# Optimization experiments

Measured on AMD Instinct MI355X. Metric: run time of the kernel, lower is better.

The kernel has to match this reference:

```python
import jax, jax.numpy as jnp
import numpy as np

N_EMBD = 1024
N_HEAD = 16
B, T = 8, 1024
EPS = 1e-5


def setup_inputs() -> dict:
    key = jax.random.key(0)
    ks = jax.random.split(key, 12)
    C = N_EMBD
    s_in = 1.0 / np.sqrt(C)
    s_ff = 1.0 / np.sqrt(4 * C)
    inp = {
        "x": jax.random.normal(ks[0], (B, T, C), dtype=jnp.float32),
        "mask": jnp.tril(jnp.ones((T, T), dtype=jnp.int32))[None, None, :, :],
        "ln1_w": jnp.ones((C,), jnp.float32),
        "ln1_b": jnp.zeros((C,), jnp.float32),
        "ln2_w": jnp.ones((C,), jnp.float32),
        "ln2_b": jnp.zeros((C,), jnp.float32),
        "wq": jax.random.normal(ks[1], (C, C), jnp.float32) * s_in,
        "bq": jnp.zeros((C,), jnp.float32),
        "wk": jax.random.normal(ks[2], (C, C), jnp.float32) * s_in,
        "bk": jnp.zeros((C,), jnp.float32),
        "wv": jax.random.normal(ks[3], (C, C), jnp.float32) * s_in,
        "bv": jnp.zeros((C,), jnp.float32),
        "wo": jax.random.normal(ks[4], (C, C), jnp.float32) * s_in,
        "bo": jnp.zeros((C,), jnp.float32),
        "w1": jax.random.normal(ks[5], (C, 4 * C), jnp.float32) * s_in,
        "b1": jnp.zeros((4 * C,), jnp.float32),
        "w2": jax.random.normal(ks[6], (4 * C, C), jnp.float32) * s_ff,
        "b2": jnp.zeros((C,), jnp.float32),
    }
    return inp


def _layer_norm(x, w, b):
    mu = jnp.mean(x, axis=-1, keepdims=True)
    var = jnp.mean(jnp.square(x - mu), axis=-1, keepdims=True)
    return (x - mu) * jax.lax.rsqrt(var + EPS) * w + b


def reference(x, mask, ln1_w, ln1_b, ln2_w, ln2_b,
              wq, bq, wk, bk, wv, bv, wo, bo, w1, b1, w2, b2):
    Bx, Tx, C = x.shape
    H = N_HEAD
    d = C // H
    h = _layer_norm(x, ln1_w, ln1_b)
    q = (h @ wq + bq).reshape(Bx, Tx, H, d)
    k = (h @ wk + bk).reshape(Bx, Tx, H, d)
    v = (h @ wv + bv).reshape(Bx, Tx, H, d)
    # [B,H,Tq,Tk] scores, scaled by sqrt(head_dim)
    scores = jnp.einsum('bqhd,bkhd->bhqk', q, k) / jnp.sqrt(jnp.float32(d))
    scores = jnp.where(mask == 0, -jnp.inf, scores)
    attn = jax.nn.softmax(scores, axis=-1)
    ctx = jnp.einsum('bhqk,bkhd->bqhd', attn, v).reshape(Bx, Tx, C)
    x = x + (ctx @ wo + bo)
    h2 = _layer_norm(x, ln2_w, ln2_b)
    ff = jax.nn.gelu(h2 @ w1 + b1, approximate=False) @ w2 + b2
    return x + ff
```

## Files before the change

kernel.cpp:

```cpp
#include <hip/hip_runtime.h>
#include <hip/hip_bf16.h>
#include <math.h>


#define DEVI __device__ __forceinline__

typedef __attribute__((ext_vector_type(4))) float floatx4;
typedef __attribute__((ext_vector_type(8))) short shortx8;

DEVI ushort f2b(float f) {
    __hip_bfloat16 h = __float2bfloat16(f);
    return __builtin_bit_cast(ushort, h);
}

DEVI void gl_lds16(const ushort* g, ushort* l) {
    __builtin_amdgcn_global_load_lds(
        (const __attribute__((address_space(1))) void*)g,
        (__attribute__((address_space(3))) void*)l, 16, 0, 0);
}

DEVI float gelu_f(float v) {
    const float u0 = 0.7978845608f * v * (1.0f + 0.044715f * v * v);
    const float u  = fminf(fmaxf(u0, -15.0f), 15.0f);
    const float e  = exp2f(u * 2.885390082f);
    const float th = 1.0f - 2.0f / (e + 1.0f);
    return 0.5f * v * (1.0f + th);
}

__global__ void transp4_kernel(const float* __restrict__ s0, const float* __restrict__ s1,
                               const float* __restrict__ s2, const float* __restrict__ s3,
                               ushort* __restrict__ d0, ushort* __restrict__ d1,
                               ushort* __restrict__ d2, ushort* __restrict__ d3) {
    const int z = blockIdx.z;
    const float* src = (z == 0) ? s0 : (z == 1) ? s1 : (z == 2) ? s2 : s3;
    ushort*      dst = (z == 0) ? d0 : (z == 1) ? d1 : (z == 2) ? d2 : d3;
    __shared__ float tile[32][33];
    const int c0 = blockIdx.x * 32, r0 = blockIdx.y * 32;
    const int tx = threadIdx.x, ty = threadIdx.y;
#pragma unroll
    for (int i = 0; i < 32; i += 8)
        tile[ty + i][tx] = src[(size_t)(r0 + ty + i) * 1024 + c0 + tx];
    __syncthreads();
#pragma unroll
    for (int i = 0; i < 32; i += 8)
        dst[(size_t)(c0 + ty + i) * 1024 + r0 + tx] = f2b(tile[tx][ty + i]);
}

__global__ void transp_kernel(const float* __restrict__ src,
                              ushort* __restrict__ dst, int R, int C) {
    __shared__ float tile[32][33];
    const int c0 = blockIdx.x * 32, r0 = blockIdx.y * 32;
    const int tx = threadIdx.x, ty = threadIdx.y;
#pragma unroll
    for (int i = 0; i < 32; i += 8)
        tile[ty + i][tx] = src[(size_t)(r0 + ty + i) * C + c0 + tx];
    __syncthreads();
#pragma unroll
    for (int i = 0; i < 32; i += 8)
        dst[(size_t)(c0 + ty + i) * R + r0 + tx] = f2b(tile[tx][ty + i]);
}

__global__ __launch_bounds__(256)
void ln_kernel(const float* __restrict__ x, const float* __restrict__ w,
               const float* __restrict__ b, ushort* __restrict__ out) {
    __shared__ float red[8];
    const int m = blockIdx.x;
    const int tid = threadIdx.x;
    const float4 xv = *(const float4*)&x[(size_t)m * 1024 + tid * 4];
    float s  = xv.x + xv.y + xv.z + xv.w;
    float s2 = xv.x * xv.x + xv.y * xv.y + xv.z * xv.z + xv.w * xv.w;
#pragma unroll
    for (int o = 32; o >= 1; o >>= 1) {
        s  += __shfl_xor(s, o, 64);
        s2 += __shfl_xor(s2, o, 64);
    }
    const int wv_ = tid >> 6;
    if ((tid & 63) == 0) { red[wv_] = s; red[4 + wv_] = s2; }
    __syncthreads();
    s  = red[0] + red[1] + red[2] + red[3];
    s2 = red[4] + red[5] + red[6] + red[7];
    const float mu   = s * (1.0f / 1024.0f);
    const float var  = s2 * (1.0f / 1024.0f) - mu * mu;
    const float rstd = rsqrtf(var + 1e-5f);
    const float4 wv = *(const float4*)&w[tid * 4];
    const float4 bv = *(const float4*)&b[tid * 4];
    ushort o4[4];
    o4[0] = f2b((xv.x - mu) * rstd * wv.x + bv.x);
    o4[1] = f2b((xv.y - mu) * rstd * wv.y + bv.y);
    o4[2] = f2b((xv.z - mu) * rstd * wv.z + bv.z);
    o4[3] = f2b((xv.w - mu) * rstd * wv.w + bv.w);
    *(uint2*)&out[(size_t)m * 1024 + tid * 4] = *(uint2*)o4;
}

template <int MODE>
__global__ __launch_bounds__(512, 4)
void gemmW(const ushort* __restrict__ A, const ushort* __restrict__ Bt,
           const float* __restrict__ biasQ, const float* __restrict__ biasK,
           const float* __restrict__ biasV,
           void* __restrict__ out, void* __restrict__ out2, void* __restrict__ out3,
           int N, int K) {
    __shared__ __align__(128) ushort lds[24576];

    const int tid  = threadIdx.x;
    const int lane = tid & 63;
    const int w    = tid >> 6;
    const int wr   = w >> 1;
    const int wc   = w & 1;

    int bx = blockIdx.x, by = blockIdx.y;
    {
        const int nwg = gridDim.x * gridDim.y;
        if ((nwg & 7) == 0) {
            const int flat = by * gridDim.x + bx;
            const int cpx  = nwg >> 3;
            const int wg   = (flat & 7) * cpx + (flat >> 3);
            bx = wg % gridDim.x;
            by = wg / gridDim.x;
        }
    }
    const int m0 = by * 256;
    const int n0 = bx * 128;

    floatx4 acc[4][4] = {};

    const int lr3 = lane >> 3;
    const int sc  = (lane & 7) ^ lr3;
    const ushort* pA = A  + (size_t)(m0 + w * 32 + lr3) * K + sc * 8;
    const ushort* pB = Bt + (size_t)(n0 + w * 16 + lr3) * K + sc * 8;
    ushort* sAd = lds + w * 2048;
    ushort* sBd = lds + 16384 + w * 1024;
    const size_t k8 = (size_t)8 * K, k16 = (size_t)16 * K, k24 = (size_t)24 * K;

    const int c0f  = (lane >> 4) ^ (lane & 7);
    const int aIdx = (wr * 64 + (lane & 15)) * 64 + c0f * 8;
    const int bIdx = (wc * 64 + (lane & 15)) * 64 + c0f * 8;
    const ushort* ar0 = lds + aIdx;
    const ushort* ar1 = lds + (aIdx ^ 32);
    const ushort* br0 = lds + 16384 + bIdx;
    const ushort* br1 = lds + 16384 + (bIdx ^ 32);

    for (int k0 = 0; k0 < K; k0 += 64) {
        __syncthreads();
        gl_lds16(pA + k0,       sAd);
        gl_lds16(pA + k8  + k0, sAd + 512);
        gl_lds16(pA + k16 + k0, sAd + 1024);
        gl_lds16(pA + k24 + k0, sAd + 1536);
        gl_lds16(pB + k0,       sBd);
        gl_lds16(pB + k8  + k0, sBd + 512);
        asm volatile("s_waitcnt vmcnt(0)" ::: "memory");
        __syncthreads();

        shortx8 af[4][2], bf[4][2];
#pragma unroll
        for (int mi = 0; mi < 4; ++mi) {
            af[mi][0] = *(const shortx8*)&ar0[mi * 1024];
            af[mi][1] = *(const shortx8*)&ar1[mi * 1024];
        }
#pragma unroll
        for (int ni = 0; ni < 4; ++ni) {
            bf[ni][0] = *(const shortx8*)&br0[ni * 1024];
            bf[ni][1] = *(const shortx8*)&br1[ni * 1024];
        }
#pragma unroll
        for (int mi = 0; mi < 4; ++mi)
#pragma unroll
            for (int ni = 0; ni < 4; ++ni) {
                acc[mi][ni] = __builtin_amdgcn_mfma_f32_16x16x32_bf16(
                    af[mi][0], bf[ni][0], acc[mi][ni], 0, 0, 0);
                acc[mi][ni] = __builtin_amdgcn_mfma_f32_16x16x32_bf16(
                    af[mi][1], bf[ni][1], acc[mi][ni], 0, 0, 0);
            }
    }
    __syncthreads();

    const int colL  = wc * 64 + (lane & 15);
    const int rbase = (wr & 1) * 64 + ((lane >> 4) << 2);
    const int mqme  = wr >> 1;

    if constexpr (MODE == 3) {
        float bvals[4];
#pragma unroll
        for (int ni = 0; ni < 4; ++ni) bvals[ni] = biasQ[n0 + colL + ni * 16];
        ushort* T = lds;
        ushort* o = (ushort*)out;
#pragma unroll
        for (int mq = 0; mq < 2; ++mq) {
            if (mqme == mq) {
#pragma unroll
                for (int mi = 0; mi < 4; ++mi)
#pragma unroll
                for (int ni = 0; ni < 4; ++ni) {
                    const int t0 = rbase + mi * 16;
#pragma unroll
                    for (int r = 0; r < 4; ++r)
                        T[(t0 + r) * 136 + colL + ni * 16] =
                            f2b(gelu_f(acc[mi][ni][r] + bvals[ni]));
                }
            }
            __syncthreads();
#pragma unroll
            for (int it = 0; it < 4; ++it) {
                const int idx = it * 512 + tid;
                const int row = idx >> 4, ch = idx & 15;
                const uint4 vv = *(const uint4*)&T[row * 136 + ch * 8];
                *(uint4*)&o[(size_t)(m0 + mq * 128 + row) * N + n0 + ch * 8] = vv;
            }
            __syncthreads();
        }
    }

    if constexpr (MODE == 1) {
        const int mat   = n0 >> 10;
        const int bb    = m0 >> 10;
        const int tbase = m0 & 1023;
        if (mat < 2) {
            const float* bp = (mat == 0) ? biasQ : biasK;
            ushort* dst = (mat == 0) ? (ushort*)out : (ushort*)out2;
            const int cb = n0 & 1023;
            float bvals[4];
#pragma unroll
            for (int ni = 0; ni < 4; ++ni) bvals[ni] = bp[cb + colL + ni * 16];
            ushort* T = lds;
#pragma unroll
            for (int mq = 0; mq < 2; ++mq) {
                if (mqme == mq) {
#pragma unroll
                    for (int mi = 0; mi < 4; ++mi)
#pragma unroll
                    for (int ni = 0; ni < 4; ++ni) {
                        const int t0 = rbase + mi * 16;
#pragma unroll
                        for (int r = 0; r < 4; ++r)
                            T[(t0 + r) * 136 + colL + ni * 16] =
                                f2b(acc[mi][ni][r] + bvals[ni]);
                    }
                }
                __syncthreads();
#pragma unroll
                for (int it = 0; it < 4; ++it) {
                    const int idx = it * 512 + tid;
                    const int row = idx >> 4, ch = idx & 15;
                    const uint4 vv = *(const uint4*)&T[row * 136 + ch * 8];
                    *(uint4*)&dst[(size_t)(m0 + mq * 128 + row) * 1024 + cb + ch * 8] = vv;
                }
                __syncthreads();
            }
        } else {
            const int vb = n0 - 2048;
            ushort* T = lds;
            ushort* Vt = (ushort*)out3;
            float bvals[4];
#pragma unroll
            for (int ni = 0; ni < 4; ++ni) bvals[ni] = biasV[vb + colL + ni * 16];
#pragma unroll
            for (int mq = 0; mq < 2; ++mq) {
                if (mqme == mq) {
#pragma unroll
                    for (int ni = 0; ni < 4; ++ni)
#pragma unroll
                    for (int mi = 0; mi < 4; ++mi) {
                        const int t0 = rbase + mi * 16;
#pragma unroll
                        for (int r = 0; r < 4; ++r)
                            T[(colL + ni * 16) * 136 + t0 + r] =
                                f2b(acc[mi][ni][r] + bvals[ni]);
                    }
                }
                __syncthreads();
#pragma unroll
                for (int it = 0; it < 4; ++it) {
                    const int idx = it * 512 + tid;
                    const int dim = idx >> 4, ch = idx & 15;
                    const uint4 vv = *(const uint4*)&T[dim * 136 + ch * 8];
                    const int d  = vb + dim;
                    const int hh = d >> 6, dl = d & 63;
                    *(uint4*)&Vt[((size_t)(bb * 16 + hh) * 64 + dl) * 1024
                                 + tbase + mq * 128 + ch * 8] = vv;
                }
                __syncthreads();
            }
        }
    }
}

__global__ __launch_bounds__(256, 4)
void gemm97r(const ushort* __restrict__ A, const ushort* __restrict__ Bt,
             const float* __restrict__ bias, float* __restrict__ out,
             const float* __restrict__ resid, int N, int K) {
    __shared__ __align__(128) ushort lds[18432];

    const int tid  = threadIdx.x;
    const int lane = tid & 63;
    const int w    = tid >> 6;
    const int wr   = w >> 1;
    const int wc   = w & 1;

    int bx = blockIdx.x, by = blockIdx.y;
    {
        const int nwg = gridDim.x * gridDim.y;
        if ((nwg & 7) == 0) {
            const int flat = by * gridDim.x + bx;
            const int cpx  = nwg >> 3;
            const int wg   = (flat & 7) * cpx + (flat >> 3);
            bx = wg % gridDim.x;
            by = wg / gridDim.x;
        }
    }
    const int m0 = by * 128;
    const int n0 = bx * 128;

    floatx4 acc[4][4] = {};

    const int lr3 = lane >> 3;
    const int sc  = (lane & 7) ^ lr3;
    const ushort* pA = A  + (size_t)(m0 + w * 32 + lr3) * K + sc * 8;
    const ushort* pB = Bt + (size_t)(n0 + w * 32 + lr3) * K + sc * 8;
    ushort* sAd = lds + w * 2048;
    ushort* sBd = lds + 8192 + w * 2048;
    const size_t k8 = (size_t)8 * K, k16 = (size_t)16 * K, k24 = (size_t)24 * K;

    const int c0f = (lane >> 4) ^ (lane & 7);
    const int aIdx = (wr * 64 + (lane & 15)) * 64 + c0f * 8;
    const int bIdx = (wc * 64 + (lane & 15)) * 64 + c0f * 8;
    const ushort* ar0 = lds + aIdx;
    const ushort* ar1 = lds + (aIdx ^ 32);
    const ushort* br0 = lds + 8192 + bIdx;
    const ushort* br1 = lds + 8192 + (bIdx ^ 32);

    for (int k0 = 0; k0 < K; k0 += 64) {
        __syncthreads();
        gl_lds16(pA + k0,       sAd);
        gl_lds16(pA + k8  + k0, sAd + 512);
        gl_lds16(pA + k16 + k0, sAd + 1024);
        gl_lds16(pA + k24 + k0, sAd + 1536);
        gl_lds16(pB + k0,       sBd);
        gl_lds16(pB + k8  + k0, sBd + 512);
        gl_lds16(pB + k16 + k0, sBd + 1024);
        gl_lds16(pB + k24 + k0, sBd + 1536);
        asm volatile("s_waitcnt vmcnt(0)" ::: "memory");
        __syncthreads();

        shortx8 af[4][2], bf[4][2];
#pragma unroll
        for (int mi = 0; mi < 4; ++mi) {
            af[mi][0] = *(const shortx8*)&ar0[mi * 1024];
            af[mi][1] = *(const shortx8*)&ar1[mi * 1024];
        }
#pragma unroll
        for (int ni = 0; ni < 4; ++ni) {
            bf[ni][0] = *(const shortx8*)&br0[ni * 1024];
            bf[ni][1] = *(const shortx8*)&br1[ni * 1024];
        }
#pragma unroll
        for (int mi = 0; mi < 4; ++mi)
#pragma unroll
            for (int ni = 0; ni < 4; ++ni) {
                acc[mi][ni] = __builtin_amdgcn_mfma_f32_16x16x32_bf16(
                    af[mi][0], bf[ni][0], acc[mi][ni], 0, 0, 0);
                acc[mi][ni] = __builtin_amdgcn_mfma_f32_16x16x32_bf16(
                    af[mi][1], bf[ni][1], acc[mi][ni], 0, 0, 0);
            }
    }
    __syncthreads();

    const int colL  = wc * 64 + (lane & 15);
    const int rbase = wr * 64 + ((lane >> 4) << 2);
    float bvals[4];
#pragma unroll
    for (int ni = 0; ni < 4; ++ni) bvals[ni] = bias[n0 + colL + ni * 16];
    float* T = (float*)lds;
    float* o = (float*)out;
#pragma unroll
    for (int half = 0; half < 2; ++half) {
        if (wr == half) {
#pragma unroll
            for (int mi = 0; mi < 4; ++mi)
#pragma unroll
            for (int ni = 0; ni < 4; ++ni) {
                const int t0 = mi * 16 + ((lane >> 4) << 2);
#pragma unroll
                for (int r = 0; r < 4; ++r)
                    T[(t0 + r) * 132 + colL + ni * 16] =
                        acc[mi][ni][r] + bvals[ni];
            }
        }
        __syncthreads();
#pragma unroll
        for (int it = 0; it < 8; ++it) {
            const int idx = it * 256 + tid;
            const int row = idx >> 5, ch = idx & 31;
            float4 tv = *(const float4*)&T[row * 132 + ch * 4];
            const size_t go = (size_t)(m0 + half * 64 + row) * N + n0 + ch * 4;
            const float4 rv = *(const float4*)&resid[go];
            tv.x += rv.x; tv.y += rv.y; tv.z += rv.z; tv.w += rv.w;
            *(float4*)&o[go] = tv;
        }
        __syncthreads();
    }
}

__global__ __launch_bounds__(256)
void attn_kernel(const ushort* __restrict__ Q, const ushort* __restrict__ Kk,
                 const ushort* __restrict__ Vt, ushort* __restrict__ ctx) {
    __shared__ ushort sK[64 * 64];
    __shared__ ushort sV[64 * 64];
    __shared__ ushort sP[4][16 * 72];

    const int tid  = threadIdx.x;
    const int lane = tid & 63;
    const int wave = tid >> 6;
    const int quad = lane >> 4;
    const int l15  = lane & 15;

    const int qb = 15 - (blockIdx.x >> 7);
    const int bh = blockIdx.x & 127;
    const size_t vbase = (size_t)bh << 16;
    const int bb = bh >> 4, h = bh & 15;

    const int lrow = lane >> 3;
    const int scb  = (lane & 7) ^ lrow;
    const ushort* Kg = Kk + ((size_t)bb * 1024 + wave * 8 + lrow) * 1024 + h * 64 + scb * 8;
    const ushort* Vg = Vt + vbase + (size_t)(wave * 8 + lrow) * 1024 + scb * 8;

    const int qrow = bb * 1024 + qb * 64 + wave * 16 + l15;
    const shortx8 qf0 = *(const shortx8*)&Q[(size_t)qrow * 1024 + h * 64 + quad * 8];
    const shortx8 qf1 = *(const shortx8*)&Q[(size_t)qrow * 1024 + h * 64 + 32 + quad * 8];

    const float SC = 0.125f * 1.44269504f;

    float mstate[4], lstate[4];
    floatx4 oacc[4] = {};
#pragma unroll
    for (int r = 0; r < 4; ++r) { mstate[r] = -__builtin_inff(); lstate[r] = 0.0f; }

    for (int kt = 0; kt <= qb; ++kt) {
        __syncthreads();
#pragma unroll
        for (int p = 0; p < 2; ++p) {
            gl_lds16(Kg + (size_t)kt * 65536 + (size_t)p * 32768,
                     sK + (p * 32 + wave * 8) * 64);
            gl_lds16(Vg + (size_t)kt * 64 + (size_t)p * 32 * 1024,
                     sV + (p * 32 + wave * 8) * 64);
        }
        __syncthreads();

        floatx4 s[4];
#pragma unroll
        for (int nt = 0; nt < 4; ++nt) {
            const int r = nt * 16 + l15;
            const int c0 = quad ^ (r & 7);
            const int c1 = (4 + quad) ^ (r & 7);
            const shortx8 kf0 = *(const shortx8*)&sK[r * 64 + c0 * 8];
            const shortx8 kf1 = *(const shortx8*)&sK[r * 64 + c1 * 8];
            floatx4 z = {};
            z = __builtin_amdgcn_mfma_f32_16x16x32_bf16(qf0, kf0, z, 0, 0, 0);
            z = __builtin_amdgcn_mfma_f32_16x16x32_bf16(qf1, kf1, z, 0, 0, 0);
            s[nt] = z;
        }
#pragma unroll
        for (int nt = 0; nt < 4; ++nt)
#pragma unroll
            for (int r = 0; r < 4; ++r) {
                float sv = s[nt][r] * SC;
                if (kt == qb) {
                    const int col = nt * 16 + l15;
                    const int row = wave * 16 + quad * 4 + r;
                    if (col > row) sv = -__builtin_inff();
                }
                s[nt][r] = sv;
            }
        float mnew[4], alpha[4];
#pragma unroll
        for (int r = 0; r < 4; ++r) {
            float mt = fmaxf(fmaxf(s[0][r], s[1][r]), fmaxf(s[2][r], s[3][r]));
#pragma unroll
            for (int o = 8; o >= 1; o >>= 1) mt = fmaxf(mt, __shfl_xor(mt, o, 64));
            mnew[r]  = fmaxf(mstate[r], mt);
            alpha[r] = exp2f(mstate[r] - mnew[r]);
            mstate[r] = mnew[r];
        }
#pragma unroll
        for (int r = 0; r < 4; ++r) {
            float rs = 0.0f;
#pragma unroll
            for (int nt = 0; nt < 4; ++nt) {
                const float p = exp2f(s[nt][r] - mnew[r]);
                s[nt][r] = p;
                rs += p;
            }
#pragma unroll
            for (int o = 8; o >= 1; o >>= 1) rs += __shfl_xor(rs, o, 64);
            lstate[r] = alpha[r] * lstate[r] + rs;
#pragma unroll
            for (int dt = 0; dt < 4; ++dt) oacc[dt][r] *= alpha[r];
        }
#pragma unroll
        for (int nt = 0; nt < 4; ++nt)
#pragma unroll
            for (int r = 0; r < 4; ++r)
                sP[wave][(quad * 4 + r) * 72 + nt * 16 + l15] = f2b(s[nt][r]);
        __asm__ volatile("s_waitcnt lgkmcnt(0)" ::: "memory");
        const shortx8 pf0 = *(const shortx8*)&sP[wave][l15 * 72 + quad * 8];
        const shortx8 pf1 = *(const shortx8*)&sP[wave][l15 * 72 + 32 + quad * 8];
#pragma unroll
        for (int dt = 0; dt < 4; ++dt) {
            const int r = dt * 16 + l15;
            const int c0 = quad ^ (r & 7);
            const int c1 = (4 + quad) ^ (r & 7);
            const shortx8 v0 = *(const shortx8*)&sV[r * 64 + c0 * 8];
            const shortx8 v1 = *(const shortx8*)&sV[r * 64 + c1 * 8];
            oacc[dt] = __builtin_amdgcn_mfma_f32_16x16x32_bf16(pf0, v0, oacc[dt], 0, 0, 0);
            oacc[dt] = __builtin_amdgcn_mfma_f32_16x16x32_bf16(pf1, v1, oacc[dt], 0, 0, 0);
        }
    }
#pragma unroll
    for (int dt = 0; dt < 4; ++dt)
#pragma unroll
        for (int r = 0; r < 4; ++r) {
            const int t = qb * 64 + wave * 16 + quad * 4 + r;
            const int dim = dt * 16 + l15;
            const float v = oacc[dt][r] / lstate[r];
            ctx[(size_t)(bb * 1024 + t) * 1024 + h * 64 + dim] = f2b(v);
        }
}

extern "C" void kernel_launch(void* const* d_in, const int* in_sizes, int n_in,
                              void* d_out, int out_size, void* d_ws, size_t ws_size,
                              hipStream_t stream) {
    const float* x    = (const float*)d_in[0];
    const float* ln1w = (const float*)d_in[2];
    const float* ln1b = (const float*)d_in[3];
    const float* ln2w = (const float*)d_in[4];
    const float* ln2b = (const float*)d_in[5];
    const float* wq   = (const float*)d_in[6];
    const float* bq   = (const float*)d_in[7];
    const float* wk   = (const float*)d_in[8];
    const float* bk   = (const float*)d_in[9];
    const float* wv   = (const float*)d_in[10];
    const float* bv   = (const float*)d_in[11];
    const float* wo   = (const float*)d_in[12];
    const float* bo   = (const float*)d_in[13];
    const float* w1   = (const float*)d_in[14];
    const float* b1   = (const float*)d_in[15];
    const float* w2   = (const float*)d_in[16];
    const float* b2   = (const float*)d_in[17];

    char* ws = (char*)d_ws;
    const size_t MB = 1024 * 1024;
    ushort* WQKVT = (ushort*)(ws + 0 * MB);
    ushort* WOT   = (ushort*)(ws + 6 * MB);
    ushort* W1T   = (ushort*)(ws + 8 * MB);
    ushort* W2T   = (ushort*)(ws + 16 * MB);
    ushort* H1    = (ushort*)(ws + 24 * MB);
    ushort* H2    = H1;
    ushort* Qb    = (ushort*)(ws + 40 * MB);
    ushort* Kb    = (ushort*)(ws + 56 * MB);
    ushort* Vbt   = (ushort*)(ws + 72 * MB);
    ushort* FF1   = (ushort*)(ws + 40 * MB);
    ushort* CTX   = (ushort*)(ws + 104 * MB);

    float* xout = (float*)d_out;

    const dim3 tb(32, 8);
    transp4_kernel<<<dim3(32, 32, 4), tb, 0, stream>>>(
        wq, wk, wv, wo,
        WQKVT, WQKVT + 1024 * 1024, WQKVT + 2048 * 1024, WOT);
    transp_kernel<<<dim3(128, 32), tb, 0, stream>>>(w1, W1T, 1024, 4096);
    transp_kernel<<<dim3(32, 128), tb, 0, stream>>>(w2, W2T, 4096, 1024);

    ln_kernel<<<8192, 256, 0, stream>>>(x, ln1w, ln1b, H1);

    gemmW<1><<<dim3(24, 32), 512, 0, stream>>>(H1, WQKVT, bq, bk, bv,
                                               Qb, Kb, Vbt, 3072, 1024);

    attn_kernel<<<2048, 256, 0, stream>>>(Qb, Kb, Vbt, CTX);

    gemm97r<<<dim3(8, 64), 256, 0, stream>>>(CTX, WOT, bo, xout, x, 1024, 1024);

    ln_kernel<<<8192, 256, 0, stream>>>(xout, ln2w, ln2b, H2);

    gemmW<3><<<dim3(32, 32), 512, 0, stream>>>(H2, W1T, b1, nullptr, nullptr,
                                               FF1, nullptr, nullptr, 4096, 1024);

    gemm97r<<<dim3(8, 64), 256, 0, stream>>>(FF1, W2T, b2, xout, xout, 1024, 4096);

    (void)in_sizes; (void)n_in; (void)out_size; (void)ws_size;
}
```

Measured before the change: 468.2 us.

## Shrink wide GEMM tiles to 128x128 and double-buffer K/V loads in attention

The QKV and FFN1 GEMMs move from 512-thread 256x128 tiles to 256-thread 128x128 tiles. This doubles the grid and removes the two-pass epilogue staging through LDS. Separately, the attention kernel now double-buffers its K and V tiles in LDS, prefetching the next key block while the current one is computed, which removes a barrier per iteration. The cost is more A/B reloads from the smaller GEMM tiles and twice the attention LDS footprint, which may lower occupancy.

```diff
diff --git a/kernel.cpp b/kernel.cpp
--- a/kernel.cpp
+++ b/kernel.cpp
@@ -93,13 +93,13 @@
 }
 
 template <int MODE>
-__global__ __launch_bounds__(512, 4)
-void gemmW(const ushort* __restrict__ A, const ushort* __restrict__ Bt,
-           const float* __restrict__ biasQ, const float* __restrict__ biasK,
-           const float* __restrict__ biasV,
-           void* __restrict__ out, void* __restrict__ out2, void* __restrict__ out3,
-           int N, int K) {
-    __shared__ __align__(128) ushort lds[24576];
+__global__ __launch_bounds__(256, 4)
+void gemm97(const ushort* __restrict__ A, const ushort* __restrict__ Bt,
+            const float* __restrict__ biasQ, const float* __restrict__ biasK,
+            const float* __restrict__ biasV,
+            void* __restrict__ out, void* __restrict__ out2, void* __restrict__ out3,
+            int N, int K) {
+    __shared__ __align__(128) ushort lds[18432];
 
     const int tid  = threadIdx.x;
     const int lane = tid & 63;
@@ -118,7 +118,7 @@
             by = wg / gridDim.x;
         }
     }
-    const int m0 = by * 256;
+    const int m0 = by * 128;
     const int n0 = bx * 128;
 
     floatx4 acc[4][4] = {};
@@ -126,18 +126,18 @@
     const int lr3 = lane >> 3;
     const int sc  = (lane & 7) ^ lr3;
     const ushort* pA = A  + (size_t)(m0 + w * 32 + lr3) * K + sc * 8;
-    const ushort* pB = Bt + (size_t)(n0 + w * 16 + lr3) * K + sc * 8;
+    const ushort* pB = Bt + (size_t)(n0 + w * 32 + lr3) * K + sc * 8;
     ushort* sAd = lds + w * 2048;
-    ushort* sBd = lds + 16384 + w * 1024;
+    ushort* sBd = lds + 8192 + w * 2048;
     const size_t k8 = (size_t)8 * K, k16 = (size_t)16 * K, k24 = (size_t)24 * K;
 
-    const int c0f  = (lane >> 4) ^ (lane & 7);
+    const int c0f = (lane >> 4) ^ (lane & 7);
     const int aIdx = (wr * 64 + (lane & 15)) * 64 + c0f * 8;
     const int bIdx = (wc * 64 + (lane & 15)) * 64 + c0f * 8;
     const ushort* ar0 = lds + aIdx;
     const ushort* ar1 = lds + (aIdx ^ 32);
-    const ushort* br0 = lds + 16384 + bIdx;
-    const ushort* br1 = lds + 16384 + (bIdx ^ 32);
+    const ushort* br0 = lds + 8192 + bIdx;
+    const ushort* br1 = lds + 8192 + (bIdx ^ 32);
 
     for (int k0 = 0; k0 < K; k0 += 64) {
         __syncthreads();
@@ -147,6 +147,8 @@
         gl_lds16(pA + k24 + k0, sAd + 1536);
         gl_lds16(pB + k0,       sBd);
         gl_lds16(pB + k8  + k0, sBd + 512);
+        gl_lds16(pB + k16 + k0, sBd + 1024);
+        gl_lds16(pB + k24 + k0, sBd + 1536);
         asm volatile("s_waitcnt vmcnt(0)" ::: "memory");
         __syncthreads();
 
@@ -174,38 +176,31 @@
     __syncthreads();
 
     const int colL  = wc * 64 + (lane & 15);
-    const int rbase = (wr & 1) * 64 + ((lane >> 4) << 2);
-    const int mqme  = wr >> 1;
+    const int rbase = wr * 64 + ((lane >> 4) << 2);
 
     if constexpr (MODE == 3) {
         float bvals[4];
 #pragma unroll
         for (int ni = 0; ni < 4; ++ni) bvals[ni] = biasQ[n0 + colL + ni * 16];
         ushort* T = lds;
+#pragma unroll
+        for (int mi = 0; mi < 4; ++mi)
+#pragma unroll
+        for (int ni = 0; ni < 4; ++ni) {
+            const int t0 = rbase + mi * 16;
+#pragma unroll
+            for (int r = 0; r < 4; ++r)
+                T[(t0 + r) * 136 + colL + ni * 16] =
+                    f2b(gelu_f(acc[mi][ni][r] + bvals[ni]));
+        }
+        __syncthreads();
         ushort* o = (ushort*)out;
 #pragma unroll
-        for (int mq = 0; mq < 2; ++mq) {
-            if (mqme == mq) {
-#pragma unroll
-                for (int mi = 0; mi < 4; ++mi)
-#pragma unroll
-                for (int ni = 0; ni < 4; ++ni) {
-                    const int t0 = rbase + mi * 16;
-#pragma unroll
-                    for (int r = 0; r < 4; ++r)
-                        T[(t0 + r) * 136 + colL + ni * 16] =
-                            f2b(gelu_f(acc[mi][ni][r] + bvals[ni]));
-                }
-            }
-            __syncthreads();
-#pragma unroll
-            for (int it = 0; it < 4; ++it) {
-                const int idx = it * 512 + tid;
-                const int row = idx >> 4, ch = idx & 15;
-                const uint4 vv = *(const uint4*)&T[row * 136 + ch * 8];
-                *(uint4*)&o[(size_t)(m0 + mq * 128 + row) * N + n0 + ch * 8] = vv;
-            }
-            __syncthreads();
+        for (int it = 0; it < 8; ++it) {
+            const int idx = it * 256 + tid;
+            const int row = idx >> 4, ch = idx & 15;
+            const uint4 vv = *(const uint4*)&T[row * 136 + ch * 8];
+            *(uint4*)&o[(size_t)(m0 + row) * N + n0 + ch * 8] = vv;
         }
     }
 
@@ -222,62 +217,48 @@
             for (int ni = 0; ni < 4; ++ni) bvals[ni] = bp[cb + colL + ni * 16];
             ushort* T = lds;
 #pragma unroll
-            for (int mq = 0; mq < 2; ++mq) {
-                if (mqme == mq) {
-#pragma unroll
-                    for (int mi = 0; mi < 4; ++mi)
-#pragma unroll
-                    for (int ni = 0; ni < 4; ++ni) {
-                        const int t0 = rbase + mi * 16;
-#pragma unroll
-                        for (int r = 0; r < 4; ++r)
-                            T[(t0 + r) * 136 + colL + ni * 16] =
-                                f2b(acc[mi][ni][r] + bvals[ni]);
-                    }
-                }
-                __syncthreads();
-#pragma unroll
-                for (int it = 0; it < 4; ++it) {
-                    const int idx = it * 512 + tid;
-                    const int row = idx >> 4, ch = idx & 15;
-                    const uint4 vv = *(const uint4*)&T[row * 136 + ch * 8];
-                    *(uint4*)&dst[(size_t)(m0 + mq * 128 + row) * 1024 + cb + ch * 8] = vv;
-                }
-                __syncthreads();
+            for (int mi = 0; mi < 4; ++mi)
+#pragma unroll
+            for (int ni = 0; ni < 4; ++ni) {
+                const int t0 = rbase + mi * 16;
+#pragma unroll
+                for (int r = 0; r < 4; ++r)
+                    T[(t0 + r) * 136 + colL + ni * 16] =
+                        f2b(acc[mi][ni][r] + bvals[ni]);
+            }
+            __syncthreads();
+#pragma unroll
+            for (int it = 0; it < 8; ++it) {
+                const int idx = it * 256 + tid;
+                const int row = idx >> 4, ch = idx & 15;
+                const uint4 vv = *(const uint4*)&T[row * 136 + ch * 8];
+                *(uint4*)&dst[(size_t)(m0 + row) * 1024 + cb + ch * 8] = vv;
             }
         } else {
             const int vb = n0 - 2048;
             ushort* T = lds;
             ushort* Vt = (ushort*)out3;
-            float bvals[4];
-#pragma unroll
-            for (int ni = 0; ni < 4; ++ni) bvals[ni] = biasV[vb + colL + ni * 16];
-#pragma unroll
-            for (int mq = 0; mq < 2; ++mq) {
-                if (mqme == mq) {
-#pragma unroll
-                    for (int ni = 0; ni < 4; ++ni)
-#pragma unroll
-                    for (int mi = 0; mi < 4; ++mi) {
-                        const int t0 = rbase + mi * 16;
-#pragma unroll
-                        for (int r = 0; r < 4; ++r)
-                            T[(colL + ni * 16) * 136 + t0 + r] =
-                                f2b(acc[mi][ni][r] + bvals[ni]);
-                    }
+#pragma unroll
+            for (int ni = 0; ni < 4; ++ni) {
+                const float bv = biasV[vb + colL + ni * 16];
+#pragma unroll
+                for (int mi = 0; mi < 4; ++mi) {
+                    const int t0 = rbase + mi * 16;
+#pragma unroll
+                    for (int r = 0; r < 4; ++r)
+                        T[(colL + ni * 16) * 136 + t0 + r] =
+                            f2b(acc[mi][ni][r] + bv);
                 }
-                __syncthreads();
-#pragma unroll
-                for (int it = 0; it < 4; ++it) {
-                    const int idx = it * 512 + tid;
-                    const int dim = idx >> 4, ch = idx & 15;
-                    const uint4 vv = *(const uint4*)&T[dim * 136 + ch * 8];
-                    const int d  = vb + dim;
-                    const int hh = d >> 6, dl = d & 63;
-                    *(uint4*)&Vt[((size_t)(bb * 16 + hh) * 64 + dl) * 1024
-                                 + tbase + mq * 128 + ch * 8] = vv;
-                }
-                __syncthreads();
+            }
+            __syncthreads();
+#pragma unroll
+            for (int it = 0; it < 8; ++it) {
+                const int idx = it * 256 + tid;
+                const int dim = idx >> 4, ch = idx & 15;
+                const uint4 vv = *(const uint4*)&T[dim * 136 + ch * 8];
+                const int d  = vb + dim;
+                const int hh = d >> 6, dl = d & 63;
+                *(uint4*)&Vt[((size_t)(bb * 16 + hh) * 64 + dl) * 1024 + tbase + ch * 8] = vv;
             }
         }
     }
@@ -402,8 +383,8 @@
 __global__ __launch_bounds__(256)
 void attn_kernel(const ushort* __restrict__ Q, const ushort* __restrict__ Kk,
                  const ushort* __restrict__ Vt, ushort* __restrict__ ctx) {
-    __shared__ ushort sK[64 * 64];
-    __shared__ ushort sV[64 * 64];
+    __shared__ ushort sK[2][64 * 64];
+    __shared__ ushort sV[2][64 * 64];
     __shared__ ushort sP[4][16 * 72];
 
     const int tid  = threadIdx.x;
@@ -433,16 +414,28 @@
 #pragma unroll
     for (int r = 0; r < 4; ++r) { mstate[r] = -__builtin_inff(); lstate[r] = 0.0f; }
 
+#pragma unroll
+    for (int p = 0; p < 2; ++p) {
+        gl_lds16(Kg + (size_t)p * 32768, sK[0] + (p * 32 + wave * 8) * 64);
+        gl_lds16(Vg + (size_t)p * 32 * 1024, sV[0] + (p * 32 + wave * 8) * 64);
+    }
+
     for (int kt = 0; kt <= qb; ++kt) {
-        __syncthreads();
-#pragma unroll
-        for (int p = 0; p < 2; ++p) {
-            gl_lds16(Kg + (size_t)kt * 65536 + (size_t)p * 32768,
-                     sK + (p * 32 + wave * 8) * 64);
-            gl_lds16(Vg + (size_t)kt * 64 + (size_t)p * 32 * 1024,
-                     sV + (p * 32 + wave * 8) * 64);
-        }
-        __syncthreads();
+        const int b = kt & 1;
+        asm volatile("s_waitcnt vmcnt(0)" ::: "memory");
+        __syncthreads();
+        if (kt < qb) {
+            const int nb = b ^ 1;
+#pragma unroll
+            for (int p = 0; p < 2; ++p) {
+                gl_lds16(Kg + (size_t)(kt + 1) * 65536 + (size_t)p * 32768,
+                         sK[nb] + (p * 32 + wave * 8) * 64);
+                gl_lds16(Vg + (size_t)(kt + 1) * 64 + (size_t)p * 32 * 1024,
+                         sV[nb] + (p * 32 + wave * 8) * 64);
+            }
+        }
+        const ushort* sKb = sK[b];
+        const ushort* sVb = sV[b];
 
         floatx4 s[4];
 #pragma unroll
@@ -450,8 +443,8 @@
             const int r = nt * 16 + l15;
             const int c0 = quad ^ (r & 7);
             const int c1 = (4 + quad) ^ (r & 7);
-            const shortx8 kf0 = *(const shortx8*)&sK[r * 64 + c0 * 8];
-            const shortx8 kf1 = *(const shortx8*)&sK[r * 64 + c1 * 8];
+            const shortx8 kf0 = *(const shortx8*)&sKb[r * 64 + c0 * 8];
+            const shortx8 kf1 = *(const shortx8*)&sKb[r * 64 + c1 * 8];
             floatx4 z = {};
             z = __builtin_amdgcn_mfma_f32_16x16x32_bf16(qf0, kf0, z, 0, 0, 0);
             z = __builtin_amdgcn_mfma_f32_16x16x32_bf16(qf1, kf1, z, 0, 0, 0);
@@ -507,8 +500,8 @@
             const int r = dt * 16 + l15;
             const int c0 = quad ^ (r & 7);
             const int c1 = (4 + quad) ^ (r & 7);
-            const shortx8 v0 = *(const shortx8*)&sV[r * 64 + c0 * 8];
-            const shortx8 v1 = *(const shortx8*)&sV[r * 64 + c1 * 8];
+            const shortx8 v0 = *(const shortx8*)&sVb[r * 64 + c0 * 8];
+            const shortx8 v1 = *(const shortx8*)&sVb[r * 64 + c1 * 8];
             oacc[dt] = __builtin_amdgcn_mfma_f32_16x16x32_bf16(pf0, v0, oacc[dt], 0, 0, 0);
             oacc[dt] = __builtin_amdgcn_mfma_f32_16x16x32_bf16(pf1, v1, oacc[dt], 0, 0, 0);
         }
@@ -570,8 +563,8 @@
 
     ln_kernel<<<8192, 256, 0, stream>>>(x, ln1w, ln1b, H1);
 
-    gemmW<1><<<dim3(24, 32), 512, 0, stream>>>(H1, WQKVT, bq, bk, bv,
-                                               Qb, Kb, Vbt, 3072, 1024);
+    gemm97<1><<<dim3(24, 64), 256, 0, stream>>>(H1, WQKVT, bq, bk, bv,
+                                                Qb, Kb, Vbt, 3072, 1024);
 
     attn_kernel<<<2048, 256, 0, stream>>>(Qb, Kb, Vbt, CTX);
 
@@ -579,8 +572,8 @@
 
     ln_kernel<<<8192, 256, 0, stream>>>(xout, ln2w, ln2b, H2);
 
-    gemmW<3><<<dim3(32, 32), 512, 0, stream>>>(H2, W1T, b1, nullptr, nullptr,
-                                               FF1, nullptr, nullptr, 4096, 1024);
+    gemm97<3><<<dim3(32, 64), 256, 0, stream>>>(H2, W1T, b1, nullptr, nullptr,
+                                                FF1, nullptr, nullptr, 4096, 1024);
 
     gemm97r<<<dim3(8, 64), 256, 0, stream>>>(FF1, W2T, b2, xout, xout, 1024, 4096);
 
```

Result: slower. 509.8 us (+8.9%).
